# Optimization experiments

Hardware: AMD Instinct MI355X
Metric: run time of the kernel (lower is better)

## Reference

```python
import jax, jax.numpy as jnp
import numpy as np

DIM = 1024
HEADS = 8
HEAD_DIM = DIM // HEADS
D_STATE = 256
BATCH = 8192
DT_MIN = 1e-3
DT_MAX = 1e-1
EPS = 1e-4  # RMSNorm eps


def setup_inputs() -> dict:
    key = jax.random.key(0)
    ks = jax.random.split(key, 8)
    x_t = jax.random.normal(ks[0], (BATCH, DIM), dtype=jnp.float32)
    state_re = jax.random.normal(ks[1], (BATCH, HEADS, D_STATE), dtype=jnp.float32)
    state_im = jax.random.normal(ks[2], (BATCH, HEADS, D_STATE), dtype=jnp.float32)
    # parameters (match torch init)
    norm_weight = jnp.ones((DIM,), dtype=jnp.float32)
    A_re_log = jnp.full((HEADS, D_STATE), float(np.log(0.5)), dtype=jnp.float32)
    n = jnp.arange(1, D_STATE + 1, dtype=jnp.float32)
    A_im = jnp.broadcast_to(float(np.pi) * n, (HEADS, D_STATE)).astype(jnp.float32)
    b_scale = 1.0 / float(np.sqrt(HEAD_DIM))
    c_scale = 1.0 / float(np.sqrt(D_STATE))
    B_re = jax.random.normal(ks[3], (HEADS, D_STATE, HEAD_DIM), dtype=jnp.float32) * b_scale
    B_im = jax.random.normal(ks[4], (HEADS, D_STATE, HEAD_DIM), dtype=jnp.float32) * b_scale
    C_re = jax.random.normal(ks[5], (HEADS, HEAD_DIM, D_STATE), dtype=jnp.float32) * c_scale
    C_im = jax.random.normal(ks[6], (HEADS, HEAD_DIM, D_STATE), dtype=jnp.float32) * c_scale
    D = jnp.ones((DIM,), dtype=jnp.float32)
    # log_dt: inverse-softplus of log-uniform dt in [dt_min, dt_max]
    u = jax.random.uniform(ks[7], (HEADS, D_STATE), dtype=jnp.float32)
    dt = jnp.exp(u * (np.log(DT_MAX) - np.log(DT_MIN)) + np.log(DT_MIN))
    dt = jnp.maximum(dt, 1e-4)
    log_dt = dt + jnp.log(-jnp.expm1(-dt))
    return dict(x_t=x_t, state_re=state_re, state_im=state_im,
                norm_weight=norm_weight, A_re_log=A_re_log, A_im=A_im,
                B_re=B_re, B_im=B_im, C_re=C_re, C_im=C_im, D=D, log_dt=log_dt)


def reference(x_t, state_re, state_im, norm_weight, A_re_log, A_im,
              B_re, B_im, C_re, C_im, D, log_dt):
    batch = x_t.shape[0]
    # RMSNorm (eps=1e-4, elementwise affine)
    ms = jnp.mean(jnp.square(x_t), axis=-1, keepdims=True)
    x = x_t * jax.lax.rsqrt(ms + EPS) * norm_weight
    x_h = x.reshape(batch, HEADS, HEAD_DIM)  # (B,H,P)
    # discretize
    A = jax.lax.complex(-jnp.exp(A_re_log), A_im)            # (H,N)
    dt = jax.nn.softplus(log_dt)                              # (H,N)
    A_bar = jnp.exp(dt.astype(A.dtype) * A)                   # (H,N) complex
    B = jax.lax.complex(B_re, B_im)                           # (H,N,P)
    C = jax.lax.complex(C_re, C_im)                           # (H,P,N)
    B_bar = ((A_bar - 1.0) / A)[..., None] * B                # (H,N,P)
    # recurrent step
    state = jax.lax.complex(state_re, state_im)               # (B,H,N)
    Bx = jnp.einsum('hnp,bhp->bhn', B_bar, x_h.astype(B_bar.dtype))
    new_state = A_bar[None] * state + Bx                      # (B,H,N)
    Ch = jnp.einsum('hpn,bhn->bhp', C, new_state)             # (B,H,P)
    D_h = D.reshape(HEADS, HEAD_DIM)[None]                    # (1,H,P)
    y_h = 2.0 * Ch.real + D_h * x_h
    out = x_t + y_h.reshape(batch, DIM)
    return out, new_state.real, new_state.imag
```

## Files before the change

### kernel.cpp

```cpp
#include <hip/hip_runtime.h>

#define BATCH 8192
#define DIM 1024
#define HEADS 8
#define HEAD_DIM 128
#define DSTATE 256

typedef __attribute__((ext_vector_type(8))) short short8v;
typedef __attribute__((ext_vector_type(4))) float f32x4;
typedef __attribute__((ext_vector_type(4))) unsigned short ushort4v;
typedef __attribute__((ext_vector_type(4))) unsigned int uint4v;

__device__ __forceinline__ unsigned short f2bf(float x) {
  unsigned int u = __builtin_bit_cast(unsigned int, x);
  unsigned int r = u + 0x7FFFu + ((u >> 16) & 1u);
  return (unsigned short)(r >> 16);
}
__device__ __forceinline__ float bf2f(unsigned short h) {
  unsigned int u = ((unsigned int)h) << 16;
  return __builtin_bit_cast(float, u);
}

__device__ __forceinline__ void stage16f(const float* g, float* l) {
  __builtin_amdgcn_global_load_lds(
      (const __attribute__((address_space(1))) unsigned int*)g,
      (__attribute__((address_space(3))) unsigned int*)l, 16, 0, 0);
}
__device__ __forceinline__ void stage4f(const float* g, float* l) {
  __builtin_amdgcn_global_load_lds(
      (const __attribute__((address_space(1))) unsigned int*)g,
      (__attribute__((address_space(3))) unsigned int*)l, 4, 0, 0);
}

#define BARRIER() do { \
  asm volatile("s_waitcnt lgkmcnt(0)" ::: "memory"); \
  __builtin_amdgcn_s_barrier(); \
  asm volatile("" ::: "memory"); } while (0)


__global__ __launch_bounds__(256) void prep(
    const float* __restrict__ logdt, const float* __restrict__ arelog,
    const float* __restrict__ aim,
    const float* __restrict__ Bre, const float* __restrict__ Bim,
    const float* __restrict__ Cre, const float* __restrict__ Cim,
    const float* __restrict__ xtg, const float* __restrict__ normw,
    unsigned short* __restrict__ w1re, unsigned short* __restrict__ w1im,
    unsigned short* __restrict__ w2re, unsigned short* __restrict__ w2mi,
    float* __restrict__ abr, float* __restrict__ abi,
    float* __restrict__ scale) {
  const int blk = blockIdx.x;
  if (blk < 1024) {
    const int i = blk * 256 + threadIdx.x;
    const int p = i & 127, s = (i >> 7) & 255, h = i >> 15;
    const int kk = s >> 4, u = s & 15;
    const int n = ((kk >> 1) << 5) + ((u >> 2) & 3) * 8 + (kk & 1) * 4 + (u & 3);
    const int hn = h * 256 + n;
    const float ld = logdt[hn];
    const float dt = log1pf(expf(ld));
    const float Ar = -expf(arelog[hn]);
    const float Ai = aim[hn];
    const float e = expf(dt * Ar), th = dt * Ai;
    const float Abr = e * cosf(th), Abi = e * sinf(th);
    if (p == 0) { abr[h * 256 + s] = Abr; abi[h * 256 + s] = Abi; }
    const float den = Ar * Ar + Ai * Ai;
    const float br_ = Abr - 1.0f;
    const float cr = (br_ * Ar + Abi * Ai) / den;
    const float ci = (Abi * Ar - br_ * Ai) / den;
    const int src = hn * 128 + p;
    const float wb = normw[h * 128 + p];
    const float bre = Bre[src], bim = Bim[src];
    w1re[i] = f2bf((cr * bre - ci * bim) * wb);
    w1im[i] = f2bf((cr * bim + ci * bre) * wb);
  } else if (blk < 2048) {
    const int i = (blk - 1024) * 256 + threadIdx.x;
    w2re[i] = f2bf(Cre[i]);
    w2mi[i] = f2bf(-Cim[i]);
  } else {
    const int wid = threadIdx.x >> 6, lane = threadIdx.x & 63;
    const int row = (blk - 2048) * 4 + wid;
    const float* xr = xtg + (size_t)row * DIM;
    float ssq = 0.f;
    #pragma unroll
    for (int c = 0; c < 4; ++c) {
      const f32x4 v = *(const f32x4*)(xr + c * 256 + lane * 4);
      ssq += v[0]*v[0] + v[1]*v[1] + v[2]*v[2] + v[3]*v[3];
    }
    #pragma unroll
    for (int m = 1; m < 64; m <<= 1) ssq += __shfl_xor(ssq, m, 64);
    if (lane == 0) scale[row] = rsqrtf(ssq * (1.0f / DIM) + 1e-4f);
  }
}

__global__ __launch_bounds__(512, 2) void s5_main(
    const unsigned short* __restrict__ w1re, const unsigned short* __restrict__ w1im,
    const unsigned short* __restrict__ w2re, const unsigned short* __restrict__ w2mi,
    const float* __restrict__ abrp, const float* __restrict__ abip,
    const float* __restrict__ scale,
    const float* __restrict__ sre, const float* __restrict__ sim,
    const float* __restrict__ xt, const float* __restrict__ dvec,
    const float* __restrict__ normw,
    float* __restrict__ out, float* __restrict__ nsre, float* __restrict__ nsim) {
  __shared__ float Sb[3][2][16][256];
  __shared__ float xtl[3][16][128];
  __shared__ unsigned short pf[2][8][64][8];
  __shared__ float scL[3][64];
  const int tid = threadIdx.x;
  const int w = tid >> 6, lane = tid & 63;
  const int g = lane >> 4, bl = lane & 15;
  const int h = blockIdx.x & 7;
  const int blkrow = (blockIdx.x >> 3) * 256;

  short8v w1r[2][4], w1i[2][4];
  #pragma unroll
  for (int t = 0; t < 2; ++t) {
    const int kk = 2 * w + t;
    const unsigned short* pr = w1re + ((size_t)(h * DSTATE + kk * 16 + bl)) * HEAD_DIM + g * 8;
    const unsigned short* pi = w1im + ((size_t)(h * DSTATE + kk * 16 + bl)) * HEAD_DIM + g * 8;
    #pragma unroll
    for (int ks = 0; ks < 4; ++ks) {
      w1r[t][ks] = *(const short8v*)(pr + ks * 32);
      w1i[t][ks] = *(const short8v*)(pi + ks * 32);
    }
  }
  short8v w2r[8], w2i[8];
  {
    const unsigned short* qr = w2re + ((size_t)(h * HEAD_DIM + w * 16 + bl)) * DSTATE + g * 8;
    const unsigned short* qi = w2mi + ((size_t)(h * HEAD_DIM + w * 16 + bl)) * DSTATE + g * 8;
    #pragma unroll
    for (int j = 0; j < 8; ++j) {
      w2r[j] = *(const short8v*)(qr + j * 32);
      w2i[j] = *(const short8v*)(qi + j * 32);
    }
  }
  f32x4 Arh[2], Aih[2];
  #pragma unroll
  for (int t = 0; t < 2; ++t) {
    Arh[t] = *(const f32x4*)(abrp + h * DSTATE + (2 * w + t) * 16 + g * 4);
    Aih[t] = *(const f32x4*)(abip + h * DSTATE + (2 * w + t) * 16 + g * 4);
  }
  f32x4 d4;
  {
    const int col = h * HEAD_DIM + w * 16 + g * 4;
    const f32x4 dv = *(const f32x4*)(dvec + col);
    const f32x4 nv = *(const f32x4*)(normw + col);
    #pragma unroll
    for (int r = 0; r < 4; ++r) d4[r] = dv[r] * nv[r];
  }

  auto STAGE = [&](int t, int b3) {
    const int gr0 = blkrow + t * 16;
    #pragma unroll
    for (int i = 0; i < 2; ++i) {
      const int row = 2 * w + i;
      const size_t rb = ((size_t)(gr0 + row) * HEADS + h) * DSTATE;
      const int soff = (lane ^ (row & 7)) * 4;
      stage16f(sre + rb + soff, &Sb[b3][0][row][0]);
      stage16f(sim + rb + soff, &Sb[b3][1][row][0]);
    }
    {
      const int row = 2 * w + (lane >> 5);
      const int soff = ((lane & 31) ^ (row & 7)) * 4;
      const float* src = xt + (size_t)(gr0 + row) * DIM + h * HEAD_DIM + soff;
      stage16f(src, &xtl[b3][2 * w][0]);
    }
    stage4f(scale + gr0 + (lane & 15), &scL[b3][0]);
  };

  STAGE(0, 0);
  STAGE(1, 1);

  for (int t = 0; t < 16; ++t) {
    const int bcur = t % 3;
    if (t < 2) { asm volatile("s_waitcnt vmcnt(6)"  ::: "memory"); }
    else       { asm volatile("s_waitcnt vmcnt(10)" ::: "memory"); }
    BARRIER();

    if (t + 2 < 16) STAGE(t + 2, (t + 2) % 3);

    const float scl = scL[bcur][bl];
    short8v xf[4];
    #pragma unroll
    for (int ks = 0; ks < 4; ++ks) {
      const f32x4 x0 = *(const f32x4*)&xtl[bcur][bl][(((ks * 8 + 2 * g)     ^ (bl & 7)) << 2)];
      const f32x4 x1 = *(const f32x4*)&xtl[bcur][bl][(((ks * 8 + 2 * g + 1) ^ (bl & 7)) << 2)];
      uint4v uv;
      uv[0] = (unsigned)f2bf(x0[0] * scl) | ((unsigned)f2bf(x0[1] * scl) << 16);
      uv[1] = (unsigned)f2bf(x0[2] * scl) | ((unsigned)f2bf(x0[3] * scl) << 16);
      uv[2] = (unsigned)f2bf(x1[0] * scl) | ((unsigned)f2bf(x1[1] * scl) << 16);
      uv[3] = (unsigned)f2bf(x1[2] * scl) | ((unsigned)f2bf(x1[3] * scl) << 16);
      xf[ks] = __builtin_bit_cast(short8v, uv);
    }

    unsigned pr0 = 0, pr1 = 0, pi0 = 0, pi1 = 0;
    #pragma unroll
    for (int tt = 0; tt < 2; ++tt) {
      f32x4 dr = {0.f,0.f,0.f,0.f};
      f32x4 di = {0.f,0.f,0.f,0.f};
      #pragma unroll
      for (int ks = 0; ks < 4; ++ks)
        dr = __builtin_amdgcn_mfma_f32_16x16x32_bf16(w1r[tt][ks], xf[ks], dr, 0, 0, 0);
      #pragma unroll
      for (int ks = 0; ks < 4; ++ks)
        di = __builtin_amdgcn_mfma_f32_16x16x32_bf16(w1i[tt][ks], xf[ks], di, 0, 0, 0);
      const int c = (((8 * w + 2 * g + tt) ^ (bl & 7)) << 2);
      const f32x4 s_r = *(const f32x4*)&Sb[bcur][0][bl][c];
      const f32x4 s_i = *(const f32x4*)&Sb[bcur][1][bl][c];
      f32x4 nr, ni;
      #pragma unroll
      for (int r = 0; r < 4; ++r) {
        nr[r] = fmaf(Arh[tt][r], s_r[r], fmaf(-Aih[tt][r], s_i[r], dr[r]));
        ni[r] = fmaf(Arh[tt][r], s_i[r], fmaf(Aih[tt][r], s_r[r], di[r]));
      }
      *(f32x4*)&Sb[bcur][0][bl][c] = nr;
      *(f32x4*)&Sb[bcur][1][bl][c] = ni;
      unsigned lo  = (unsigned)f2bf(nr[0]) | ((unsigned)f2bf(nr[1]) << 16);
      unsigned hi  = (unsigned)f2bf(nr[2]) | ((unsigned)f2bf(nr[3]) << 16);
      unsigned lo2 = (unsigned)f2bf(ni[0]) | ((unsigned)f2bf(ni[1]) << 16);
      unsigned hi2 = (unsigned)f2bf(ni[2]) | ((unsigned)f2bf(ni[3]) << 16);
      if (tt == 0) { pr0 = lo; pr1 = hi; pi0 = lo2; pi1 = hi2; }
      else {
        uint4v urv; urv[0] = pr0; urv[1] = pr1; urv[2] = lo;  urv[3] = hi;
        uint4v uiv; uiv[0] = pi0; uiv[1] = pi1; uiv[2] = lo2; uiv[3] = hi2;
        *(short8v*)&pf[0][w][lane][0] = __builtin_bit_cast(short8v, urv);
        *(short8v*)&pf[1][w][lane][0] = __builtin_bit_cast(short8v, uiv);
      }
    }
    BARRIER();

    #pragma unroll
    for (int i = 0; i < 2; ++i) {
      const int row = 2 * w + i;
      const size_t rb = ((size_t)(blkrow + t * 16 + row) * HEADS + h) * DSTATE;
      const int gc = (lane ^ (row & 7)) * 4;
      const f32x4 vr = *(const f32x4*)&Sb[bcur][0][row][lane * 4];
      const f32x4 vi = *(const f32x4*)&Sb[bcur][1][row][lane * 4];
      *(f32x4*)(nsre + rb + gc) = vr;
      *(f32x4*)(nsim + rb + gc) = vi;
    }

    f32x4 a2 = {0.f,0.f,0.f,0.f};
    #pragma unroll
    for (int j = 0; j < 8; ++j) {
      const short8v pbr = *(const short8v*)&pf[0][j][lane][0];
      const short8v pbi = *(const short8v*)&pf[1][j][lane][0];
      a2 = __builtin_amdgcn_mfma_f32_16x16x32_bf16(w2r[j], pbr, a2, 0, 0, 0);
      a2 = __builtin_amdgcn_mfma_f32_16x16x32_bf16(w2i[j], pbi, a2, 0, 0, 0);
    }

    {
      const int col = h * HEAD_DIM + w * 16 + g * 4;
      const size_t o = (size_t)(blkrow + t * 16 + bl) * DIM + col;
      const f32x4 xt4 = *(const f32x4*)&xtl[bcur][bl][(((4 * w + g) ^ (bl & 7)) << 2)];
      f32x4 ro;
      #pragma unroll
      for (int r = 0; r < 4; ++r)
        ro[r] = xt4[r] * (1.0f + d4[r] * scl) + 2.0f * a2[r];
      *(f32x4*)(out + o) = ro;
    }
  }
}

extern "C" void kernel_launch(void* const* d_in, const int* in_sizes, int n_in,
                              void* d_out, int out_size, void* d_ws, size_t ws_size,
                              hipStream_t stream) {
  const float* x_t      = (const float*)d_in[0];
  const float* state_re = (const float*)d_in[1];
  const float* state_im = (const float*)d_in[2];
  const float* norm_w   = (const float*)d_in[3];
  const float* A_re_log = (const float*)d_in[4];
  const float* A_im     = (const float*)d_in[5];
  const float* B_re     = (const float*)d_in[6];
  const float* B_im     = (const float*)d_in[7];
  const float* C_re     = (const float*)d_in[8];
  const float* C_im     = (const float*)d_in[9];
  const float* Dv       = (const float*)d_in[10];
  const float* log_dt   = (const float*)d_in[11];

  float* out   = (float*)d_out;
  float* ns_re = out + (size_t)BATCH * DIM;
  float* ns_im = ns_re + (size_t)BATCH * HEADS * DSTATE;

  char* ws = (char*)d_ws;
  unsigned short* w1re = (unsigned short*)ws;
  unsigned short* w1im = w1re + 262144;
  unsigned short* w2re = w1im + 262144;
  unsigned short* w2mi = w2re + 262144;
  float* abr   = (float*)(ws + 4 * 524288);
  float* abi   = abr + 2048;
  float* scale = abi + 2048;

  prep<<<4096, 256, 0, stream>>>(log_dt, A_re_log, A_im, B_re, B_im, C_re, C_im,
                                 x_t, norm_w, w1re, w1im, w2re, w2mi,
                                 abr, abi, scale);
  s5_main<<<256, 512, 0, stream>>>(w1re, w1im, w2re, w2mi, abr, abi, scale,
                                   state_re, state_im, x_t, Dv, norm_w,
                                   out, ns_re, ns_im);
}
```

Baseline: 92.30 us.

## Precompute bf16 normalized x in prep and raise main-kernel occupancy

```diff
diff --git a/kernel.cpp b/kernel.cpp
--- a/kernel.cpp
+++ b/kernel.cpp
@@ -25,11 +25,6 @@
   __builtin_amdgcn_global_load_lds(
       (const __attribute__((address_space(1))) unsigned int*)g,
       (__attribute__((address_space(3))) unsigned int*)l, 16, 0, 0);
-}
-__device__ __forceinline__ void stage4f(const float* g, float* l) {
-  __builtin_amdgcn_global_load_lds(
-      (const __attribute__((address_space(1))) unsigned int*)g,
-      (__attribute__((address_space(3))) unsigned int*)l, 4, 0, 0);
 }
 
 #define BARRIER() do { \
@@ -47,7 +42,7 @@
     unsigned short* __restrict__ w1re, unsigned short* __restrict__ w1im,
     unsigned short* __restrict__ w2re, unsigned short* __restrict__ w2mi,
     float* __restrict__ abr, float* __restrict__ abi,
-    float* __restrict__ scale) {
+    float* __restrict__ rscale, unsigned short* __restrict__ xhb) {
   const int blk = blockIdx.x;
   if (blk < 1024) {
     const int i = blk * 256 + threadIdx.x;
@@ -79,36 +74,43 @@
     const int wid = threadIdx.x >> 6, lane = threadIdx.x & 63;
     const int row = (blk - 2048) * 4 + wid;
     const float* xr = xtg + (size_t)row * DIM;
+    unsigned short* xo = xhb + (size_t)row * DIM;
+    f32x4 v[4];
     float ssq = 0.f;
     #pragma unroll
     for (int c = 0; c < 4; ++c) {
-      const f32x4 v = *(const f32x4*)(xr + c * 256 + lane * 4);
-      ssq += v[0]*v[0] + v[1]*v[1] + v[2]*v[2] + v[3]*v[3];
+      v[c] = *(const f32x4*)(xr + c * 256 + lane * 4);
+      ssq += v[c][0]*v[c][0] + v[c][1]*v[c][1] + v[c][2]*v[c][2] + v[c][3]*v[c][3];
     }
     #pragma unroll
     for (int m = 1; m < 64; m <<= 1) ssq += __shfl_xor(ssq, m, 64);
-    if (lane == 0) scale[row] = rsqrtf(ssq * (1.0f / DIM) + 1e-4f);
-  }
-}
-
-__global__ __launch_bounds__(512, 2) void s5_main(
+    const float sc = rsqrtf(ssq * (1.0f / DIM) + 1e-4f);
+    if (lane == 0) rscale[row] = 1.0f / sc;
+    #pragma unroll
+    for (int c = 0; c < 4; ++c) {
+      ushort4v o;
+      o[0] = f2bf(v[c][0] * sc); o[1] = f2bf(v[c][1] * sc);
+      o[2] = f2bf(v[c][2] * sc); o[3] = f2bf(v[c][3] * sc);
+      *(ushort4v*)(xo + c * 256 + lane * 4) = o;
+    }
+  }
+}
+
+__global__ __launch_bounds__(512, 4) void s5_main(
     const unsigned short* __restrict__ w1re, const unsigned short* __restrict__ w1im,
     const unsigned short* __restrict__ w2re, const unsigned short* __restrict__ w2mi,
     const float* __restrict__ abrp, const float* __restrict__ abip,
-    const float* __restrict__ scale,
+    const float* __restrict__ rscale, const unsigned short* __restrict__ xhb,
     const float* __restrict__ sre, const float* __restrict__ sim,
-    const float* __restrict__ xt, const float* __restrict__ dvec,
-    const float* __restrict__ normw,
+    const float* __restrict__ dvec, const float* __restrict__ normw,
     float* __restrict__ out, float* __restrict__ nsre, float* __restrict__ nsim) {
-  __shared__ float Sb[3][2][16][256];
-  __shared__ float xtl[3][16][128];
+  __shared__ float Sb[2][2][16][256];
   __shared__ unsigned short pf[2][8][64][8];
-  __shared__ float scL[3][64];
   const int tid = threadIdx.x;
   const int w = tid >> 6, lane = tid & 63;
   const int g = lane >> 4, bl = lane & 15;
   const int h = blockIdx.x & 7;
-  const int blkrow = (blockIdx.x >> 3) * 256;
+  const int blkrow = (blockIdx.x >> 3) * 128;
 
   short8v w1r[2][4], w1i[2][4];
   #pragma unroll
@@ -122,75 +124,35 @@
       w1i[t][ks] = *(const short8v*)(pi + ks * 32);
     }
   }
-  short8v w2r[8], w2i[8];
-  {
-    const unsigned short* qr = w2re + ((size_t)(h * HEAD_DIM + w * 16 + bl)) * DSTATE + g * 8;
-    const unsigned short* qi = w2mi + ((size_t)(h * HEAD_DIM + w * 16 + bl)) * DSTATE + g * 8;
-    #pragma unroll
-    for (int j = 0; j < 8; ++j) {
-      w2r[j] = *(const short8v*)(qr + j * 32);
-      w2i[j] = *(const short8v*)(qi + j * 32);
-    }
-  }
   f32x4 Arh[2], Aih[2];
   #pragma unroll
   for (int t = 0; t < 2; ++t) {
     Arh[t] = *(const f32x4*)(abrp + h * DSTATE + (2 * w + t) * 16 + g * 4);
     Aih[t] = *(const f32x4*)(abip + h * DSTATE + (2 * w + t) * 16 + g * 4);
   }
-  f32x4 d4;
-  {
-    const int col = h * HEAD_DIM + w * 16 + g * 4;
-    const f32x4 dv = *(const f32x4*)(dvec + col);
-    const f32x4 nv = *(const f32x4*)(normw + col);
-    #pragma unroll
-    for (int r = 0; r < 4; ++r) d4[r] = dv[r] * nv[r];
-  }
-
-  auto STAGE = [&](int t, int b3) {
+
+  auto STAGE = [&](int t) {
+    const int b = t & 1;
     const int gr0 = blkrow + t * 16;
     #pragma unroll
     for (int i = 0; i < 2; ++i) {
       const int row = 2 * w + i;
       const size_t rb = ((size_t)(gr0 + row) * HEADS + h) * DSTATE;
       const int soff = (lane ^ (row & 7)) * 4;
-      stage16f(sre + rb + soff, &Sb[b3][0][row][0]);
-      stage16f(sim + rb + soff, &Sb[b3][1][row][0]);
-    }
+      stage16f(sre + rb + soff, &Sb[b][0][row][0]);
+      stage16f(sim + rb + soff, &Sb[b][1][row][0]);
+    }
+  };
+
+  auto PHASE1 = [&](int t) {
+    const int b = t & 1;
+    short8v xf[4];
     {
-      const int row = 2 * w + (lane >> 5);
-      const int soff = ((lane & 31) ^ (row & 7)) * 4;
-      const float* src = xt + (size_t)(gr0 + row) * DIM + h * HEAD_DIM + soff;
-      stage16f(src, &xtl[b3][2 * w][0]);
-    }
-    stage4f(scale + gr0 + (lane & 15), &scL[b3][0]);
-  };
-
-  STAGE(0, 0);
-  STAGE(1, 1);
-
-  for (int t = 0; t < 16; ++t) {
-    const int bcur = t % 3;
-    if (t < 2) { asm volatile("s_waitcnt vmcnt(6)"  ::: "memory"); }
-    else       { asm volatile("s_waitcnt vmcnt(10)" ::: "memory"); }
-    BARRIER();
-
-    if (t + 2 < 16) STAGE(t + 2, (t + 2) % 3);
-
-    const float scl = scL[bcur][bl];
-    short8v xf[4];
-    #pragma unroll
-    for (int ks = 0; ks < 4; ++ks) {
-      const f32x4 x0 = *(const f32x4*)&xtl[bcur][bl][(((ks * 8 + 2 * g)     ^ (bl & 7)) << 2)];
-      const f32x4 x1 = *(const f32x4*)&xtl[bcur][bl][(((ks * 8 + 2 * g + 1) ^ (bl & 7)) << 2)];
-      uint4v uv;
-      uv[0] = (unsigned)f2bf(x0[0] * scl) | ((unsigned)f2bf(x0[1] * scl) << 16);
-      uv[1] = (unsigned)f2bf(x0[2] * scl) | ((unsigned)f2bf(x0[3] * scl) << 16);
-      uv[2] = (unsigned)f2bf(x1[0] * scl) | ((unsigned)f2bf(x1[1] * scl) << 16);
-      uv[3] = (unsigned)f2bf(x1[2] * scl) | ((unsigned)f2bf(x1[3] * scl) << 16);
-      xf[ks] = __builtin_bit_cast(short8v, uv);
-    }
-
+      const unsigned short* xrow = xhb + (size_t)(blkrow + t * 16 + bl) * DIM + h * HEAD_DIM + g * 8;
+      #pragma unroll
+      for (int ks = 0; ks < 4; ++ks)
+        xf[ks] = *(const short8v*)(xrow + ks * 32);
+    }
     unsigned pr0 = 0, pr1 = 0, pi0 = 0, pi1 = 0;
     #pragma unroll
     for (int tt = 0; tt < 2; ++tt) {
@@ -203,16 +165,16 @@
       for (int ks = 0; ks < 4; ++ks)
         di = __builtin_amdgcn_mfma_f32_16x16x32_bf16(w1i[tt][ks], xf[ks], di, 0, 0, 0);
       const int c = (((8 * w + 2 * g + tt) ^ (bl & 7)) << 2);
-      const f32x4 s_r = *(const f32x4*)&Sb[bcur][0][bl][c];
-      const f32x4 s_i = *(const f32x4*)&Sb[bcur][1][bl][c];
+      const f32x4 s_r = *(const f32x4*)&Sb[b][0][bl][c];
+      const f32x4 s_i = *(const f32x4*)&Sb[b][1][bl][c];
       f32x4 nr, ni;
       #pragma unroll
       for (int r = 0; r < 4; ++r) {
         nr[r] = fmaf(Arh[tt][r], s_r[r], fmaf(-Aih[tt][r], s_i[r], dr[r]));
         ni[r] = fmaf(Arh[tt][r], s_i[r], fmaf(Aih[tt][r], s_r[r], di[r]));
       }
-      *(f32x4*)&Sb[bcur][0][bl][c] = nr;
-      *(f32x4*)&Sb[bcur][1][bl][c] = ni;
+      *(f32x4*)&Sb[b][0][bl][c] = nr;
+      *(f32x4*)&Sb[b][1][bl][c] = ni;
       unsigned lo  = (unsigned)f2bf(nr[0]) | ((unsigned)f2bf(nr[1]) << 16);
       unsigned hi  = (unsigned)f2bf(nr[2]) | ((unsigned)f2bf(nr[3]) << 16);
       unsigned lo2 = (unsigned)f2bf(ni[0]) | ((unsigned)f2bf(ni[1]) << 16);
@@ -225,38 +187,56 @@
         *(short8v*)&pf[1][w][lane][0] = __builtin_bit_cast(short8v, uiv);
       }
     }
-    BARRIER();
-
+  };
+
+  auto PHASE2 = [&](int t) {
+    const int b = t & 1;
     #pragma unroll
     for (int i = 0; i < 2; ++i) {
       const int row = 2 * w + i;
       const size_t rb = ((size_t)(blkrow + t * 16 + row) * HEADS + h) * DSTATE;
       const int gc = (lane ^ (row & 7)) * 4;
-      const f32x4 vr = *(const f32x4*)&Sb[bcur][0][row][lane * 4];
-      const f32x4 vi = *(const f32x4*)&Sb[bcur][1][row][lane * 4];
+      const f32x4 vr = *(const f32x4*)&Sb[b][0][row][lane * 4];
+      const f32x4 vi = *(const f32x4*)&Sb[b][1][row][lane * 4];
       *(f32x4*)(nsre + rb + gc) = vr;
       *(f32x4*)(nsim + rb + gc) = vi;
     }
-
+    const unsigned short* qr = w2re + ((size_t)(h * HEAD_DIM + w * 16 + bl)) * DSTATE + g * 8;
+    const unsigned short* qi = w2mi + ((size_t)(h * HEAD_DIM + w * 16 + bl)) * DSTATE + g * 8;
     f32x4 a2 = {0.f,0.f,0.f,0.f};
     #pragma unroll
     for (int j = 0; j < 8; ++j) {
+      const short8v a2r = *(const short8v*)(qr + j * 32);
+      const short8v a2i = *(const short8v*)(qi + j * 32);
       const short8v pbr = *(const short8v*)&pf[0][j][lane][0];
       const short8v pbi = *(const short8v*)&pf[1][j][lane][0];
-      a2 = __builtin_amdgcn_mfma_f32_16x16x32_bf16(w2r[j], pbr, a2, 0, 0, 0);
-      a2 = __builtin_amdgcn_mfma_f32_16x16x32_bf16(w2i[j], pbi, a2, 0, 0, 0);
-    }
-
-    {
-      const int col = h * HEAD_DIM + w * 16 + g * 4;
-      const size_t o = (size_t)(blkrow + t * 16 + bl) * DIM + col;
-      const f32x4 xt4 = *(const f32x4*)&xtl[bcur][bl][(((4 * w + g) ^ (bl & 7)) << 2)];
-      f32x4 ro;
-      #pragma unroll
-      for (int r = 0; r < 4; ++r)
-        ro[r] = xt4[r] * (1.0f + d4[r] * scl) + 2.0f * a2[r];
-      *(f32x4*)(out + o) = ro;
-    }
+      a2 = __builtin_amdgcn_mfma_f32_16x16x32_bf16(a2r, pbr, a2, 0, 0, 0);
+      a2 = __builtin_amdgcn_mfma_f32_16x16x32_bf16(a2i, pbi, a2, 0, 0, 0);
+    }
+    const int row = blkrow + t * 16 + bl;
+    const float rs = rscale[row];
+    const int col = h * HEAD_DIM + w * 16 + g * 4;
+    const f32x4 dv = *(const f32x4*)(dvec + col);
+    const f32x4 nv = *(const f32x4*)(normw + col);
+    const ushort4v xh4 = *(const ushort4v*)(xhb + (size_t)row * DIM + col);
+    f32x4 ro;
+    #pragma unroll
+    for (int r = 0; r < 4; ++r)
+      ro[r] = bf2f(xh4[r]) * (rs + dv[r] * nv[r]) + 2.0f * a2[r];
+    *(f32x4*)(out + (size_t)row * DIM + col) = ro;
+  };
+
+  STAGE(0);
+
+  for (int t = 0; t < 8; ++t) {
+    if (t == 0) asm volatile("s_waitcnt vmcnt(0)" ::: "memory");
+    else        asm volatile("s_waitcnt vmcnt(5)" ::: "memory");
+    BARRIER();
+    if (t + 1 < 8) STAGE(t + 1);
+    __builtin_amdgcn_sched_barrier(0);
+    PHASE1(t);
+    BARRIER();
+    PHASE2(t);
   }
 }
 
@@ -285,14 +265,15 @@
   unsigned short* w1im = w1re + 262144;
   unsigned short* w2re = w1im + 262144;
   unsigned short* w2mi = w2re + 262144;
-  float* abr   = (float*)(ws + 4 * 524288);
-  float* abi   = abr + 2048;
-  float* scale = abi + 2048;
+  float* abr    = (float*)(ws + 4 * 524288);
+  float* abi    = abr + 2048;
+  float* rscale = abi + 2048;
+  unsigned short* xhb = (unsigned short*)(rscale + 8192);
 
   prep<<<4096, 256, 0, stream>>>(log_dt, A_re_log, A_im, B_re, B_im, C_re, C_im,
                                  x_t, norm_w, w1re, w1im, w2re, w2mi,
-                                 abr, abi, scale);
-  s5_main<<<256, 512, 0, stream>>>(w1re, w1im, w2re, w2mi, abr, abi, scale,
-                                   state_re, state_im, x_t, Dv, norm_w,
+                                 abr, abi, rscale, xhb);
+  s5_main<<<512, 512, 0, stream>>>(w1re, w1im, w2re, w2mi, abr, abi, rscale, xhb,
+                                   state_re, state_im, Dv, norm_w,
                                    out, ns_re, ns_im);
 }
```

Result: slower. 184.2 us (+99.5%).
